# Kernel tuning notes

Measured on AMD Instinct MI355X. Metric: run time of the kernel, lower is better.

The kernel has to match this reference:

```python
import jax, jax.numpy as jnp
import numpy as np
from jax import lax

NUM_C = 100
EMB = 256
B = 64
L = 500
NSTU = 4096
N = NUM_C + 1  # skill_embedding rows / GCN node count


def gcn_conv(x, src, dst, W, b):
    # PyG GCNConv: add self-loops, symmetric deg^-1/2 norm, scatter-add at target.
    # x: [N, Fin]; src, dst: [E] (duplicates kept, as in PyG); W: [Fout, Fin]
    n = x.shape[0]
    loop = jnp.arange(n)
    s = jnp.concatenate([src, loop])
    d = jnp.concatenate([dst, loop])
    deg = jnp.zeros((n,), x.dtype).at[d].add(1.0)
    dinv = jnp.where(deg > 0, lax.rsqrt(deg), 0.0)
    norm = dinv[s] * dinv[d]  # [E+N]
    h = x @ W.T
    out = jnp.zeros((n, h.shape[1]), x.dtype).at[d].add(norm[:, None] * h[s])
    return out + b


def rnn(x, Wih, Whh, bih, bhh):
    # torch.nn.RNN (tanh, batch_first): h_t = tanh(x_t Wih^T + bih + h_{t-1} Whh^T + bhh)
    h0 = jnp.zeros((x.shape[0], Whh.shape[0]), x.dtype)
    def step(h, xt):
        h = jnp.tanh(xt @ Wih.T + bih + h @ Whh.T + bhh)
        return h, h
    _, hs = lax.scan(step, h0, jnp.swapaxes(x, 0, 1))
    return jnp.swapaxes(hs, 0, 1)


def next_pred(res, skill):
    # (res * one_hot(next_skill)).sum(-1); row NUM_C of the one-hot table is all-zero padding
    ns = skill[:, 1:]
    p = jnp.take_along_axis(res, jnp.minimum(ns, NUM_C - 1)[..., None], axis=-1)[..., 0]
    return jnp.where(ns == NUM_C, 0.0, p)


def _forward(student, skill, answer, G, skill_emb, answer_emb, stu,
             hg_w1, hg_b1, hg_w2, hg_b2, gcn_w1, gcn_b1, gcn_w2, gcn_b2,
             w1_w, w1_b, w2_w, w2_b, fc_d_w, fc_d_b, fc_h_w, fc_h_b,
             fc_e_w, fc_e_b, pos, dg_wih, dg_whh, dg_bih, dg_bhh,
             hgr_wih, hgr_whh, hgr_bih, hgr_bhh):
    mask = (answer != 2)[..., None].astype(jnp.float32)  # [B,L,1]
    src, dst = skill[:, :-1], skill[:, 1:]               # per-sample edge lists [B,L-1]

    # HGNN over student hypergraph (eval mode: dropout = identity): x' = G (x W + b)
    h = jax.nn.relu(G @ (stu @ hg_w1.T + hg_b1))
    stu_embedding = G @ (h @ hg_w2.T + hg_b2)            # [NSTU, EMB]

    se = skill_emb[skill]                                # [B,L,EMB]
    ae = answer_emb[answer]
    skill_answer = jnp.concatenate([se, ae], -1)
    answer_skill = jnp.concatenate([ae, se], -1)
    stu_h = stu_embedding[student - 1]                   # one_hot @ table == gather, [B,L,EMB]

    # per-sample 2-layer GCN over the shared skill embedding table, vmapped over batch
    gcn2 = jax.vmap(lambda s, d: gcn_conv(
        jax.nn.relu(gcn_conv(skill_emb, s, d, gcn_w1, gcn_b1)), s, d, gcn_w2, gcn_b2))
    all_h = gcn2(src, dst)                               # [B,N,EMB]

    g = jnp.take_along_axis(all_h, skill[..., None], axis=1) * mask  # [B,L,EMB]
    lengths = mask.sum(axis=1)[:, 0].astype(jnp.int32)   # effective lengths [B]
    expand_pos = pos[lengths - 1]                        # [B,L,1] (L==500)
    expand_pos = jax.nn.softmax(expand_pos * mask, axis=1)
    pooled = (g * expand_pos).sum(axis=1)                # [B,EMB]
    pooled = jnp.broadcast_to(pooled[:, None, :], (B, L, EMB))

    x = jnp.where((answer == 1)[..., None], skill_answer, answer_skill)  # [B,L,2E]
    h_dg = rnn(jnp.concatenate([pooled, x], -1), dg_wih, dg_whh, dg_bih, dg_bhh)
    h_hg = rnn(jnp.concatenate([stu_h, x], -1), hgr_wih, hgr_whh, hgr_bih, hgr_bhh)

    logit_h = h_hg @ fc_h_w.T + fc_h_b
    logit_d = h_dg @ fc_d_w.T + fc_d_b
    theta = jax.nn.sigmoid(h_hg @ w1_w.T + w1_b + h_dg @ w2_w.T + w2_b)
    ens = jnp.concatenate([theta * h_hg, (1.0 - theta) * h_dg], -1) @ fc_e_w.T + fc_e_b
    return (next_pred(logit_h[:, :-1], skill),
            next_pred(logit_d[:, :-1], skill),
            next_pred(ens[:, :-1], skill))


def setup_inputs() -> dict:
    key = jax.random.key(0)
    ks = jax.random.split(key, 24)
    f = lambda i, shape, s=0.05: jax.random.normal(ks[i], shape, jnp.float32) * s
    return {
        "student": jax.random.randint(ks[0], (B, L), 1, NSTU + 1),
        "skill": jax.random.randint(ks[1], (B, L), 0, N),
        "answer": jax.random.randint(ks[2], (B, L), 0, 3),
        "G": f(3, (NSTU, NSTU), 0.01),
        "skill_emb": f(4, (N, EMB), 1.0),
        "answer_emb": f(5, (3, EMB), 1.0),
        "stu": f(6, (NSTU, EMB), 1.0),
        "hg_w1": f(7, (EMB, EMB)), "hg_b1": jnp.zeros((EMB,), jnp.float32),
        "hg_w2": f(8, (EMB, EMB)), "hg_b2": jnp.zeros((EMB,), jnp.float32),
        "gcn_w1": f(9, (8, EMB)), "gcn_b1": jnp.zeros((8,), jnp.float32),
        "gcn_w2": f(10, (EMB, 8)), "gcn_b2": jnp.zeros((EMB,), jnp.float32),
        "w1_w": f(11, (EMB, EMB)), "w1_b": jnp.zeros((EMB,), jnp.float32),
        "w2_w": f(12, (EMB, EMB)), "w2_b": jnp.zeros((EMB,), jnp.float32),
        "fc_d_w": f(13, (NUM_C, EMB)), "fc_d_b": jnp.zeros((NUM_C,), jnp.float32),
        "fc_h_w": f(14, (NUM_C, EMB)), "fc_h_b": jnp.zeros((NUM_C,), jnp.float32),
        "fc_e_w": f(15, (NUM_C, 2 * EMB)), "fc_e_b": jnp.zeros((NUM_C,), jnp.float32),
        "pos": jax.random.uniform(ks[16], (500, 500, 1), jnp.float32),
        "dg_wih": f(17, (EMB, 3 * EMB)), "dg_whh": f(18, (EMB, EMB)),
        "dg_bih": jnp.zeros((EMB,), jnp.float32), "dg_bhh": jnp.zeros((EMB,), jnp.float32),
        "hgr_wih": f(19, (EMB, 3 * EMB)), "hgr_whh": f(20, (EMB, EMB)),
        "hgr_bih": jnp.zeros((EMB,), jnp.float32), "hgr_bhh": jnp.zeros((EMB,), jnp.float32),
    }


def reference(student, skill, answer, G, skill_emb, answer_emb, stu,
              hg_w1, hg_b1, hg_w2, hg_b2, gcn_w1, gcn_b1, gcn_w2, gcn_b2,
              w1_w, w1_b, w2_w, w2_b, fc_d_w, fc_d_b, fc_h_w, fc_h_b,
              fc_e_w, fc_e_b, pos, dg_wih, dg_whh, dg_bih, dg_bhh,
              hgr_wih, hgr_whh, hgr_bih, hgr_bhh):
    return _forward(student, skill, answer, G, skill_emb, answer_emb, stu,
                    hg_w1, hg_b1, hg_w2, hg_b2, gcn_w1, gcn_b1, gcn_w2, gcn_b2,
                    w1_w, w1_b, w2_w, w2_b, fc_d_w, fc_d_b, fc_h_w, fc_h_b,
                    fc_e_w, fc_e_b, pos, dg_wih, dg_whh, dg_bih, dg_bhh,
                    hgr_wih, hgr_whh, hgr_bih, hgr_bhh)
```

## Files before the change

kernel.cpp:

```cpp
#include <hip/hip_runtime.h>
#include <cstdint>
#include <cstddef>

typedef unsigned short u16;
typedef __attribute__((ext_vector_type(8))) short short8;
typedef __attribute__((ext_vector_type(4))) short short4v;
typedef __attribute__((ext_vector_type(4))) float f32x4;

__device__ __forceinline__ float b2f(u16 u){ return __uint_as_float(((unsigned)u)<<16); }
__device__ __forceinline__ u16 f2b(float f){
    unsigned u = __float_as_uint(f);
    return (u16)((u + 0x7fffu + ((u>>16)&1u)) >> 16);
}
__device__ __forceinline__ int iclamp(int v, int lo, int hi){ return v<lo?lo:(v>hi?hi:v); }

__device__ __forceinline__ void barrier_lds(){
    asm volatile("s_waitcnt lgkmcnt(0)\n\ts_barrier" ::: "memory");
}

__device__ __forceinline__ float fast_exp2(float x){
#if __has_builtin(__builtin_amdgcn_exp2f)
    return __builtin_amdgcn_exp2f(x);
#else
    return __expf(x * 0.6931471805599453f);
#endif
}

__device__ __forceinline__ short8 ld8f(const float* p){
    f32x4 a = *(const f32x4*)p;
    f32x4 b = *(const f32x4*)(p+4);
    short8 r;
    #pragma unroll
    for(int j=0;j<4;j++){ r[j]=(short)f2b(a[j]); r[4+j]=(short)f2b(b[j]); }
    return r;
}
__device__ __forceinline__ short8 ld8f_s(const float* p, float s){
    f32x4 a = *(const f32x4*)p;
    f32x4 b = *(const f32x4*)(p+4);
    short8 r;
    #pragma unroll
    for(int j=0;j<4;j++){ r[j]=(short)f2b(a[j]*s); r[4+j]=(short)f2b(b[j]*s); }
    return r;
}
__device__ __forceinline__ short8 ld8b(const u16* p){ return *(const short8*)p; }

#define C_TANH 2.8853900817779268f

template<bool TRANSOUT, bool RELU, bool AF32, bool BF32>
__global__ __launch_bounds__(256) void gemm64(
    const void* __restrict__ A, const void* __restrict__ B,
    const float* __restrict__ bias, u16* __restrict__ C,
    int M, int N, int K, int ldb, int ldc)
{
    constexpr int BK=32;
    __shared__ u16 As[2][64][BK+8];
    __shared__ u16 Bs[2][64][BK+8];
    const int tid = threadIdx.x;
    const int bm = blockIdx.x*64, bn = blockIdx.y*64;
    const int wave = tid>>6, lane = tid&63, lm = lane&15, lg = lane>>4;
    const int wm = (wave>>1)*32, wn = (wave&1)*32;
    f32x4 acc[2][2];
    #pragma unroll
    for(int i=0;i<2;i++){ acc[i][0]=(f32x4){0.f,0.f,0.f,0.f}; acc[i][1]=(f32x4){0.f,0.f,0.f,0.f}; }

    const int arow = tid>>2, akc = (tid&3)*8;
    auto lda8 = [&](int k)->short8{
        return AF32 ? ld8f((const float*)A + (size_t)(bm+arow)*K + k+akc)
                    : ld8b((const u16*)A + (size_t)(bm+arow)*K + k+akc);
    };
    auto ldb8v = [&](int k)->short8{
        return BF32 ? ld8f((const float*)B + (size_t)(bn+arow)*ldb + k+akc)
                    : ld8b((const u16*)B + (size_t)(bn+arow)*ldb + k+akc);
    };
    *(short8*)&As[0][arow][akc] = lda8(0);
    *(short8*)&Bs[0][arow][akc] = ldb8v(0);
    short8 a_hold, b_hold;
    if(BK < K){ a_hold = lda8(BK); b_hold = ldb8v(BK); }
    barrier_lds();
    int p = 0;
    for(int k0=0;k0<K;k0+=BK){
        short8 a_next, b_next;
        const bool have2 = (k0+2*BK < K);
        if(have2){ a_next = lda8(k0+2*BK); b_next = ldb8v(k0+2*BK); }
        short8 af[2], bfg[2];
        #pragma unroll
        for(int mt=0;mt<2;mt++) af[mt]  = *(const short8*)&As[p][wm+mt*16+lm][lg*8];
        #pragma unroll
        for(int nt=0;nt<2;nt++) bfg[nt] = *(const short8*)&Bs[p][wn+nt*16+lm][lg*8];
        if(k0+BK < K){
            *(short8*)&As[p^1][arow][akc] = a_hold;
            *(short8*)&Bs[p^1][arow][akc] = b_hold;
        }
        #pragma unroll
        for(int nt=0;nt<2;nt++)
            #pragma unroll
            for(int mt=0;mt<2;mt++)
                acc[mt][nt] = __builtin_amdgcn_mfma_f32_16x16x32_bf16(af[mt], bfg[nt], acc[mt][nt], 0,0,0);
        barrier_lds();
        a_hold = a_next; b_hold = b_next;
        p ^= 1;
    }
    #pragma unroll
    for(int nt=0;nt<2;nt++){
        const int col = bn+wn+nt*16+lm;
        const float bv = bias ? bias[col] : 0.f;
        #pragma unroll
        for(int mt=0;mt<2;mt++){
            const int row0 = bm+wm+mt*16+lg*4;
            #pragma unroll
            for(int r=0;r<4;r++){
                const int row = row0+r;
                float v = acc[mt][nt][r] + bv;
                if(RELU) v = fmaxf(v, 0.f);
                const size_t idx = TRANSOUT ? ((size_t)col*ldc + row) : ((size_t)row*ldc + col);
                C[idx] = f2b(v);
            }
        }
    }
}

__global__ __launch_bounds__(256) void k_prep(
    const float* __restrict__ skill_emb, const float* __restrict__ answer_emb,
    const float* __restrict__ wih_dg, const float* __restrict__ bih_dg, const float* __restrict__ bhh_dg,
    const float* __restrict__ wih_hg, const float* __restrict__ bih_hg, const float* __restrict__ bhh_hg,
    const float* __restrict__ gcn_w1,
    const int* __restrict__ skill, const int* __restrict__ answer, const int* __restrict__ student,
    const float* __restrict__ G, u16* __restrict__ Gb,
    float* __restrict__ table_dg, float* __restrict__ table_hg,
    float* __restrict__ h1pre, int* __restrict__ combo_t, int* __restrict__ sid_t)
{
    const int bid = blockIdx.x, tid = threadIdx.x;
    if(bid < 606){
        const int which = (bid >= 303) ? 1 : 0;
        const int combo = bid - which*303;
        const float* wih = which ? wih_hg : wih_dg;
        const float* bih = which ? bih_hg : bih_dg;
        const float* bhh = which ? bhh_hg : bhh_dg;
        float* table     = which ? table_hg : table_dg;
        const int sid = combo/3, ans = combo - sid*3;
        __shared__ float sf[256], sg[256];
        sf[tid] = (ans==1) ? skill_emb[(size_t)sid*256+tid] : answer_emb[(size_t)ans*256+tid];
        sg[tid] = (ans==1) ? answer_emb[(size_t)ans*256+tid] : skill_emb[(size_t)sid*256+tid];
        __syncthreads();
        const int o = tid;
        float acc = bih[o] + bhh[o];
        const float* w = wih + (size_t)o*768;
        for(int k=0;k<256;k+=4){
            f32x4 w1v = *(const f32x4*)&w[256+k];
            f32x4 w2v = *(const f32x4*)&w[512+k];
            acc += sf[k]*w1v.x + sf[k+1]*w1v.y + sf[k+2]*w1v.z + sf[k+3]*w1v.w;
            acc += sg[k]*w2v.x + sg[k+1]*w2v.y + sg[k+2]*w2v.z + sg[k+3]*w2v.w;
        }
        table[(size_t)combo*256 + o] = acc;
    } else if(bid < 731){
        const int i = (bid-606)*256 + tid;
        if(i>=32000) return;
        const int t = i>>6, b = i&63;
        const int sk = iclamp(skill[b*500+t], 0, 100);
        const int an = iclamp(answer[b*500+t], 0, 2);
        const int sd = iclamp(student[b*500+t]-1, 0, 4095);
        combo_t[i] = sk*3+an;
        sid_t[i]   = sd;
    } else if(bid < 739){
        if(tid >= 101) return;
        const int idx = (bid-731)*101 + tid;
        if(idx>=808) return;
        const int n=idx>>3, j=idx&7;
        const float* x = skill_emb + n*256;
        const float* w = gcn_w1 + j*256;
        float acc=0.f;
        for(int k=0;k<256;k+=4){
            f32x4 a = *(const f32x4*)&x[k];
            f32x4 b = *(const f32x4*)&w[k];
            acc += a.x*b.x + a.y*b.y + a.z*b.z + a.w*b.w;
        }
        h1pre[idx]=acc;
    } else {
        const size_t i = ((size_t)(bid-739)*256 + tid)*8;
        *(short8*)&Gb[i] = ld8f(G + i);
    }
}

__global__ __launch_bounds__(256) void k_gcn(
    const int* __restrict__ skill, const int* __restrict__ answer,
    const float* __restrict__ pos, const float* __restrict__ h1pre,
    const float* __restrict__ gcn_b1, const float* __restrict__ gcn_w2, const float* __restrict__ gcn_b2,
    const float* __restrict__ wih_dg,
    u16* __restrict__ pooled_proj)
{
    const int b = blockIdx.x, tid = threadIdx.x;
    __shared__ int   sk[500];
    __shared__ float msk[500];
    __shared__ float coef[500];
    __shared__ float deg[101];
    __shared__ float agg1[101*8];
    __shared__ float agg2[101*8];
    __shared__ float red[256];
    __shared__ float vec8[8];
    __shared__ float sS[1];

    for(int i=tid;i<500;i+=256){
        sk[i]=iclamp(skill[b*500+i],0,100);
        msk[i] = (answer[b*500+i]!=2)?1.f:0.f;
    }
    for(int i=tid;i<101;i+=256) deg[i]=1.f;
    if(tid<8)  vec8[tid]=0.f;
    if(tid==8) sS[0]=0.f;
    __syncthreads();
    for(int e=tid;e<499;e+=256) atomicAdd(&deg[sk[e+1]], 1.f);
    __syncthreads();
    for(int i=tid;i<101;i+=256) deg[i] = rsqrtf(deg[i]);
    float cnt=0.f; for(int i=tid;i<500;i+=256) cnt += msk[i];
    __syncthreads();
    red[tid]=cnt; __syncthreads();
    for(int s=128;s>0;s>>=1){ if(tid<s) red[tid]+=red[tid+s]; __syncthreads(); }
    const int len = iclamp((int)(red[0]+0.5f), 1, 500);
    __syncthreads();
    for(int i=tid;i<808;i+=256){ const int n=i>>3; agg1[i] = deg[n]*deg[n]*h1pre[i]; }
    __syncthreads();
    for(int i=tid;i<499*8;i+=256){
        const int e=i>>3, j=i&7, s=sk[e], d=sk[e+1];
        atomicAdd(&agg1[d*8+j], deg[s]*deg[d]*h1pre[s*8+j]);
    }
    __syncthreads();
    for(int i=tid;i<808;i+=256){ const int j=i&7; agg1[i] = fmaxf(agg1[i]+gcn_b1[j], 0.f); }
    __syncthreads();
    for(int i=tid;i<808;i+=256){ const int n=i>>3; agg2[i] = deg[n]*deg[n]*agg1[i]; }
    __syncthreads();
    for(int i=tid;i<499*8;i+=256){
        const int e=i>>3, j=i&7, s=sk[e], d=sk[e+1];
        atomicAdd(&agg2[d*8+j], deg[s]*deg[d]*agg1[s*8+j]);
    }
    const size_t prow = (size_t)(len-1)*500;
    float vmax = -1e30f;
    for(int i=tid;i<500;i+=256){ const float v = pos[prow+i]*msk[i]; coef[i]=v; vmax=fmaxf(vmax,v); }
    red[tid]=vmax; __syncthreads();
    for(int s=128;s>0;s>>=1){ if(tid<s) red[tid]=fmaxf(red[tid],red[tid+s]); __syncthreads(); }
    const float m = red[0]; __syncthreads();
    float lsum=0.f;
    for(int i=tid;i<500;i+=256){ const float e=__expf(coef[i]-m); coef[i]=e; lsum+=e; }
    red[tid]=lsum; __syncthreads();
    for(int s=128;s>0;s>>=1){ if(tid<s) red[tid]+=red[tid+s]; __syncthreads(); }
    const float inv = 1.f/red[0];
    __syncthreads();
    float v8[8]={0,0,0,0,0,0,0,0}; float ls=0.f;
    for(int i=tid;i<500;i+=256){
        const float ci = coef[i]*inv*msk[i];
        if(ci!=0.f){
            const int n=sk[i]; ls+=ci;
            #pragma unroll
            for(int j=0;j<8;j++) v8[j] += ci*agg2[n*8+j];
        }
    }
    #pragma unroll
    for(int j=0;j<8;j++) atomicAdd(&vec8[j], v8[j]);
    atomicAdd(&sS[0], ls);
    __syncthreads();
    {
        const int o = tid;
        float acc = gcn_b2[o]*sS[0];
        #pragma unroll
        for(int j=0;j<8;j++) acc += vec8[j]*gcn_w2[o*8+j];
        red[o] = acc;
    }
    __syncthreads();
    {
        const int o = tid;
        const float* w = wih_dg + (size_t)o*768;
        float acc=0.f;
        for(int k=0;k<256;k+=4){
            f32x4 wv = *(const f32x4*)&w[k];
            acc += red[k]*wv.x + red[k+1]*wv.y + red[k+2]*wv.z + red[k+3]*wv.w;
        }
        pooled_proj[b*256+o]=f2b(acc);
    }
}

__global__ __launch_bounds__(256) void k_pre(
    const int* __restrict__ combo_t, const int* __restrict__ sid_t,
    const float* __restrict__ table_dg, const float* __restrict__ table_hg,
    const u16* __restrict__ pooled_proj, const u16* __restrict__ stu_proj,
    u16* __restrict__ pre_dg, u16* __restrict__ pre_hg)
{
    const int t = blockIdx.x, rnn = blockIdx.y, c = threadIdx.x;
    const int b0 = blockIdx.z*16;
    const float* tab = rnn ? table_hg : table_dg;
    u16* outp = rnn ? pre_hg : pre_dg;
    for(int b=b0;b<b0+16;b++){
        const int cmb = combo_t[t*64+b];
        const u16* prow = rnn ? (stu_proj + (size_t)sid_t[t*64+b]*256)
                              : (pooled_proj + (size_t)b*256);
        const float v = (tab[(size_t)cmb*256 + c] + b2f(prow[c])) * C_TANH;
        outp[((size_t)t*64+b)*256 + c] = f2b(v);
    }
}

__global__ __launch_bounds__(1024) void k_rnn(
    const u16* __restrict__ pre_dg, const u16* __restrict__ pre_hg,
    const float* __restrict__ whh_dg, const float* __restrict__ whh_hg,
    u16* __restrict__ hall_dg, u16* __restrict__ hall_hg)
{
    __shared__ u16 hc[2][8][4][16][8];
    const int bid = blockIdx.x;
    const int rnn = bid>>2, grp = bid&3, rb = grp*16;
    const float* W   = rnn ? whh_hg : whh_dg;
    const u16*  pre  = rnn ? pre_hg : pre_dg;
    u16*        out  = rnn ? hall_hg : hall_dg;
    const int tid = threadIdx.x, wave = tid>>6, lane = tid&63;
    const int lm = lane&15, lg = lane>>4;
    const int cb = wave*16;

    short8 wf[8];
    #pragma unroll
    for(int kk=0;kk<8;kk++)
        wf[kk] = ld8f_s(W + (size_t)(cb+lm)*256 + kk*32 + lg*8, C_TANH);

    for(int i=tid;i<2*8*4*16*8/2;i+=1024) ((unsigned*)hc)[i]=0;

    const size_t base = (size_t)(rb+lm)*256 + cb + lg*4;
    const int wchunk = wave>>1, wsub = (wave&1)*2 + (lg>>1), wslot = (lg&1)*4;

    const u16* pp = pre + base;
    u16*       op = out + base;
    uint2 pv = *(const uint2*)pp;
    pp += 16384;
    __syncthreads();

    auto stepf = [&](const u16 (&S)[8][4][16][8], u16 (&D)[8][4][16][8],
                     uint2 pvi, const u16* ppi, u16* opi)->uint2 {
        f32x4 a0, c0 = (f32x4){0.f,0.f,0.f,0.f};
        a0[0] = __uint_as_float(pvi.x << 16);
        a0[1] = __uint_as_float(pvi.x & 0xffff0000u);
        a0[2] = __uint_as_float(pvi.y << 16);
        a0[3] = __uint_as_float(pvi.y & 0xffff0000u);
        #pragma unroll
        for(int kk=0;kk<4;kk++){
            short8 hb = *(const short8*)&S[kk][lg][lm][0];
            a0 = __builtin_amdgcn_mfma_f32_16x16x32_bf16(wf[kk], hb, a0, 0,0,0);
        }
        #pragma unroll
        for(int kk=4;kk<8;kk++){
            short8 hb = *(const short8*)&S[kk][lg][lm][0];
            c0 = __builtin_amdgcn_mfma_f32_16x16x32_bf16(wf[kk], hb, c0, 0,0,0);
        }
        const uint2 pvn = *(const uint2*)ppi;
        float th[4];
        #pragma unroll
        for(int r=0;r<4;r++){
            const float x = a0[r] + c0[r];
            const float e = fast_exp2(x);
            th[r] = fmaf(-2.f, __builtin_amdgcn_rcpf(e + 1.f), 1.f);
        }
        uint2 pk;
        asm("v_cvt_pk_bf16_f32 %0, %1, %2" : "=v"(pk.x) : "v"(th[0]), "v"(th[1]));
        asm("v_cvt_pk_bf16_f32 %0, %1, %2" : "=v"(pk.y) : "v"(th[2]), "v"(th[3]));
        *(uint2*)&D[wchunk][wsub][lm][wslot] = pk;
        *(uint2*)opi = pk;
        barrier_lds();
        return pvn;
    };

    for(int t=0;t<500;t+=2){
        pv = stepf(hc[0], hc[1], pv, pp, op);  pp += 16384; op += 16384;
        pv = stepf(hc[1], hc[0], pv, pp, op);  pp += 16384; op += 16384;
    }
}

__global__ __launch_bounds__(256) void k_theta(
    const u16* __restrict__ Ah, const u16* __restrict__ Ad,
    const float* __restrict__ w1, const float* __restrict__ w2,
    const float* __restrict__ b1, const float* __restrict__ b2,
    u16* __restrict__ theta)
{
    constexpr int BK=32;
    __shared__ u16 AsH[128][BK+8];
    __shared__ u16 AsD[128][BK+8];
    __shared__ u16 BsH[64][BK+8];
    __shared__ u16 BsD[64][BK+8];
    const int tid = threadIdx.x;
    const int bm = blockIdx.x*128, bn = blockIdx.y*64;
    const int wave = tid>>6, lane = tid&63, lm = lane&15, lg = lane>>4;
    const int wm = (wave>>1)*64, wn = (wave&1)*32;
    f32x4 acc[4][2];
    #pragma unroll
    for(int i=0;i<4;i++){ acc[i][0]=(f32x4){0.f,0.f,0.f,0.f}; acc[i][1]=(f32x4){0.f,0.f,0.f,0.f}; }

    const int arow0 = tid>>2, akc0 = (tid&3)*8;
    const int arow1 = arow0 + 64;
    for(int k0=0;k0<256;k0+=BK){
        *(short8*)&AsH[arow0][akc0] = ld8b(Ah + (size_t)(bm+arow0)*256 + k0+akc0);
        *(short8*)&AsH[arow1][akc0] = ld8b(Ah + (size_t)(bm+arow1)*256 + k0+akc0);
        *(short8*)&AsD[arow0][akc0] = ld8b(Ad + (size_t)(bm+arow0)*256 + k0+akc0);
        *(short8*)&AsD[arow1][akc0] = ld8b(Ad + (size_t)(bm+arow1)*256 + k0+akc0);
        *(short8*)&BsH[arow0][akc0] = ld8f(w1 + (size_t)(bn+arow0)*256 + k0+akc0);
        *(short8*)&BsD[arow0][akc0] = ld8f(w2 + (size_t)(bn+arow0)*256 + k0+akc0);
        __syncthreads();
        short8 afH[4], afD[4], bf1[2], bf2[2];
        #pragma unroll
        for(int mt=0;mt<4;mt++){
            afH[mt] = *(const short8*)&AsH[wm+mt*16+lm][lg*8];
            afD[mt] = *(const short8*)&AsD[wm+mt*16+lm][lg*8];
        }
        #pragma unroll
        for(int nt=0;nt<2;nt++){
            bf1[nt] = *(const short8*)&BsH[wn+nt*16+lm][lg*8];
            bf2[nt] = *(const short8*)&BsD[wn+nt*16+lm][lg*8];
        }
        #pragma unroll
        for(int nt=0;nt<2;nt++)
            #pragma unroll
            for(int mt=0;mt<4;mt++){
                acc[mt][nt] = __builtin_amdgcn_mfma_f32_16x16x32_bf16(afH[mt], bf1[nt], acc[mt][nt], 0,0,0);
                acc[mt][nt] = __builtin_amdgcn_mfma_f32_16x16x32_bf16(afD[mt], bf2[nt], acc[mt][nt], 0,0,0);
            }
        __syncthreads();
    }
    #pragma unroll
    for(int nt=0;nt<2;nt++){
        const int col = bn+wn+nt*16+lm;
        const float bb = b1[col]+b2[col];
        #pragma unroll
        for(int mt=0;mt<4;mt++){
            const int row0 = bm+wm+mt*16+lg*4;
            #pragma unroll
            for(int r=0;r<4;r++){
                const float x = acc[mt][nt][r] + bb;
                theta[(size_t)(row0+r)*256 + col] = f2b(1.f/(1.f+__expf(-x)));
            }
        }
    }
}

__global__ __launch_bounds__(256) void k_out(
    const int* __restrict__ skill,
    const u16* __restrict__ hall_hg, const u16* __restrict__ hall_dg,
    const u16* __restrict__ theta,
    const float* __restrict__ fc_h_w, const float* __restrict__ fc_h_b,
    const float* __restrict__ fc_d_w, const float* __restrict__ fc_d_b,
    const float* __restrict__ fc_e_w, const float* __restrict__ fc_e_b,
    float* __restrict__ outp)
{
    const int tid=threadIdx.x, lane=tid&63;
    const int wid = blockIdx.x*4 + (tid>>6);
    const int b = wid/499, t = wid - b*499;
    const int ns = skill[b*500 + t + 1];
    float o0=0.f,o1=0.f,o2=0.f,bh=0.f,bd=0.f,be=0.f;
    if(ns != 100){
        const int c = iclamp(ns, 0, 99);
        const size_t r = (size_t)t*64 + b;
        const int k = lane*4;
        short4v hh  = *(const short4v*)&hall_hg[r*256+k];
        short4v hd  = *(const short4v*)&hall_dg[r*256+k];
        short4v th  = *(const short4v*)&theta[r*256+k];
        f32x4 fh  = *(const f32x4*)&fc_h_w[(size_t)c*256+k];
        f32x4 fd  = *(const f32x4*)&fc_d_w[(size_t)c*256+k];
        f32x4 fe1 = *(const f32x4*)&fc_e_w[(size_t)c*512+k];
        f32x4 fe2 = *(const f32x4*)&fc_e_w[(size_t)c*512+256+k];
        #pragma unroll
        for(int j=0;j<4;j++){
            const float hhj=b2f((u16)hh[j]), hdj=b2f((u16)hd[j]), tj=b2f((u16)th[j]);
            o0 += hhj*fh[j];
            o1 += hdj*fd[j];
            o2 += tj*hhj*fe1[j] + (1.f-tj)*hdj*fe2[j];
        }
        #pragma unroll
        for(int off=32;off>0;off>>=1){
            o0 += __shfl_down(o0,off);
            o1 += __shfl_down(o1,off);
            o2 += __shfl_down(o2,off);
        }
        bh=fc_h_b[c]; bd=fc_d_b[c]; be=fc_e_b[c];
    }
    if(lane==0){
        outp[            b*499+t] = (ns==100)?0.f:(o0+bh);
        outp[31936     + b*499+t] = (ns==100)?0.f:(o1+bd);
        outp[2*31936   + b*499+t] = (ns==100)?0.f:(o2+be);
    }
}

extern "C" void kernel_launch(void* const* d_in, const int* in_sizes, int n_in,
                              void* d_out, int out_size, void* d_ws, size_t ws_size,
                              hipStream_t stream)
{
    const int* student = (const int*)d_in[0];
    const int* skill   = (const int*)d_in[1];
    const int* answer  = (const int*)d_in[2];
    const float* G        = (const float*)d_in[3];
    const float* skill_emb= (const float*)d_in[4];
    const float* answer_emb=(const float*)d_in[5];
    const float* stu      = (const float*)d_in[6];
    const float* hg_w1    = (const float*)d_in[7];
    const float* hg_b1    = (const float*)d_in[8];
    const float* hg_w2    = (const float*)d_in[9];
    const float* hg_b2    = (const float*)d_in[10];
    const float* gcn_w1   = (const float*)d_in[11];
    const float* gcn_b1   = (const float*)d_in[12];
    const float* gcn_w2   = (const float*)d_in[13];
    const float* gcn_b2   = (const float*)d_in[14];
    const float* w1_w     = (const float*)d_in[15];
    const float* w1_b     = (const float*)d_in[16];
    const float* w2_w     = (const float*)d_in[17];
    const float* w2_b     = (const float*)d_in[18];
    const float* fc_d_w   = (const float*)d_in[19];
    const float* fc_d_b   = (const float*)d_in[20];
    const float* fc_h_w   = (const float*)d_in[21];
    const float* fc_h_b   = (const float*)d_in[22];
    const float* fc_e_w   = (const float*)d_in[23];
    const float* fc_e_b   = (const float*)d_in[24];
    const float* pos      = (const float*)d_in[25];
    const float* dg_wih   = (const float*)d_in[26];
    const float* dg_whh   = (const float*)d_in[27];
    const float* dg_bih   = (const float*)d_in[28];
    const float* dg_bhh   = (const float*)d_in[29];
    const float* hgr_wih  = (const float*)d_in[30];
    const float* hgr_whh  = (const float*)d_in[31];
    const float* hgr_bih  = (const float*)d_in[32];
    const float* hgr_bhh  = (const float*)d_in[33];

    char* ws = (char*)d_ws;
    size_t off = 0;
    auto nxt = [&](size_t bytes)->char*{
        char* r = ws + off;
        off += (bytes + 255) & ~(size_t)255;
        return r;
    };
    float* h1pre      = (float*)nxt(808*4);
    float* table_dg   = (float*)nxt(303*256*4);
    float* table_hg   = (float*)nxt(303*256*4);
    u16*   tmpT       = (u16*)  nxt((size_t)256*4096*2);
    u16*   hbuf       = (u16*)  nxt((size_t)4096*256*2);
    u16*   stu_proj   = (u16*)  nxt((size_t)4096*256*2);
    u16*   pooled_proj= (u16*)  nxt(64*256*2);
    int*   combo_t    = (int*)  nxt(32000*4);
    int*   sid_t      = (int*)  nxt(32000*4);
    u16*   Gb         = (u16*)  nxt((size_t)4096*4096*2);
    u16*   hall_dg    = (u16*)  nxt((size_t)32000*256*2);
    u16*   hall_hg    = (u16*)  nxt((size_t)32000*256*2);
    u16*   pre_dg     = Gb;
    u16*   pre_hg     = Gb + (size_t)32000*256;
    u16*   theta      = pre_dg;

    k_prep<<<8931,256,0,stream>>>(skill_emb, answer_emb,
                                  dg_wih, dg_bih, dg_bhh,
                                  hgr_wih, hgr_bih, hgr_bhh,
                                  gcn_w1, skill, answer, student,
                                  G, Gb,
                                  table_dg, table_hg, h1pre, combo_t, sid_t);
    k_gcn<<<64,256,0,stream>>>(skill, answer, pos, h1pre, gcn_b1, gcn_w2, gcn_b2,
                               dg_wih, pooled_proj);

    gemm64<true ,false,true ,true ><<<dim3(64,4),256,0,stream>>>(stu,  hg_w1, hg_b1, tmpT, 4096,256,256,  256, 4096);
    gemm64<false,true ,false,false><<<dim3(64,4),256,0,stream>>>(Gb,   tmpT,  nullptr, hbuf, 4096,256,4096, 4096, 256);
    gemm64<true ,false,false,true ><<<dim3(64,4),256,0,stream>>>(hbuf, hg_w2, hg_b2, tmpT, 4096,256,256,  256, 4096);
    gemm64<false,false,false,false><<<dim3(64,4),256,0,stream>>>(Gb,   tmpT,  nullptr, hbuf, 4096,256,4096, 4096, 256);
    gemm64<false,false,false,true ><<<dim3(64,4),256,0,stream>>>(hbuf, hgr_wih, nullptr, stu_proj, 4096,256,256, 768, 256);

    k_pre<<<dim3(500,2,4),256,0,stream>>>(combo_t, sid_t, table_dg, table_hg,
                                          pooled_proj, stu_proj, pre_dg, pre_hg);

    k_rnn<<<8,1024,0,stream>>>(pre_dg, pre_hg, dg_whh, hgr_whh, hall_dg, hall_hg);

    k_theta<<<dim3(250,4),256,0,stream>>>(hall_hg, hall_dg, w1_w, w2_w, w1_b, w2_b, theta);
    k_out<<<7984,256,0,stream>>>(skill, hall_hg, hall_dg, theta,
                                 fc_h_w, fc_h_b, fc_d_w, fc_d_b, fc_e_w, fc_e_b,
                                 (float*)d_out);
}
```

Baseline: 789.6 us.

## Fuse HGNN GEMM chain and pre-activation gather into one persistent kernel

Replaces the five separate GEMM launches and the k_pre launch with a single 256-block persistent kernel. Stages are separated by a global atomic-counter barrier, and the counter is reset inside k_prep. The intent is to remove kernel launch gaps and tail effects between the dependent stages. In exchange, the pre-activation gather now runs as a 250-iteration serial loop per block instead of thousands of blocks, which cuts latency hiding. The global barrier also relies on all 256 blocks being co-resident on the device.

```diff
diff --git a/kernel.cpp b/kernel.cpp
--- a/kernel.cpp
+++ b/kernel.cpp
@@ -46,17 +46,29 @@
 
 #define C_TANH 2.8853900817779268f
 
+__device__ __forceinline__ void gsync(unsigned* cnt, unsigned target){
+    __syncthreads();
+    __threadfence();
+    if(threadIdx.x==0){
+        atomicAdd(cnt, 1u);
+        while(__hip_atomic_load(cnt, __ATOMIC_RELAXED, __HIP_MEMORY_SCOPE_AGENT) < target){
+            __builtin_amdgcn_s_sleep(2);
+        }
+    }
+    __syncthreads();
+    __threadfence();
+}
+
 template<bool TRANSOUT, bool RELU, bool AF32, bool BF32>
-__global__ __launch_bounds__(256) void gemm64(
+__device__ __forceinline__ void gemm_dev(
     const void* __restrict__ A, const void* __restrict__ B,
     const float* __restrict__ bias, u16* __restrict__ C,
-    int M, int N, int K, int ldb, int ldc)
+    int M, int N, int K, int ldb, int ldc, int bx, int by,
+    u16 (&As)[2][64][40], u16 (&Bs)[2][64][40])
 {
     constexpr int BK=32;
-    __shared__ u16 As[2][64][BK+8];
-    __shared__ u16 Bs[2][64][BK+8];
     const int tid = threadIdx.x;
-    const int bm = blockIdx.x*64, bn = blockIdx.y*64;
+    const int bm = bx*64, bn = by*64;
     const int wave = tid>>6, lane = tid&63, lm = lane&15, lg = lane>>4;
     const int wm = (wave>>1)*32, wn = (wave&1)*32;
     f32x4 acc[2][2];
@@ -119,6 +131,49 @@
     }
 }
 
+__global__ __launch_bounds__(256) void k_mega(
+    const float* __restrict__ stu, const float* __restrict__ hg_w1, const float* __restrict__ hg_b1,
+    const u16* __restrict__ Gb, const float* __restrict__ hg_w2, const float* __restrict__ hg_b2,
+    const float* __restrict__ hgr_wih,
+    u16* __restrict__ tmpT, u16* __restrict__ hbuf, u16* __restrict__ stu_proj,
+    const int* __restrict__ combo_t, const int* __restrict__ sid_t,
+    const float* __restrict__ table_dg, const float* __restrict__ table_hg,
+    const u16* __restrict__ pooled_proj,
+    u16* __restrict__ pre_dg, u16* __restrict__ pre_hg,
+    unsigned* __restrict__ cnt)
+{
+    __shared__ u16 As[2][64][40];
+    __shared__ u16 Bs[2][64][40];
+    const int bid = blockIdx.x;
+    const int bx = bid & 63, by = bid >> 6;
+
+    gemm_dev<true ,false,true ,true >(stu,  hg_w1, hg_b1, tmpT, 4096,256,256,  256, 4096, bx,by, As,Bs);
+    gsync(cnt, 256);
+    gemm_dev<false,true ,false,false>(Gb,   tmpT,  nullptr, hbuf, 4096,256,4096, 4096, 256, bx,by, As,Bs);
+    gsync(cnt, 512);
+    gemm_dev<true ,false,false,true >(hbuf, hg_w2, hg_b2, tmpT, 4096,256,256,  256, 4096, bx,by, As,Bs);
+    gsync(cnt, 768);
+    gemm_dev<false,false,false,false>(Gb,   tmpT,  nullptr, hbuf, 4096,256,4096, 4096, 256, bx,by, As,Bs);
+    gsync(cnt, 1024);
+    gemm_dev<false,false,false,true >(hbuf, hgr_wih, nullptr, stu_proj, 4096,256,256, 768, 256, bx,by, As,Bs);
+    gsync(cnt, 1280);
+
+    const int c = threadIdx.x;
+    int tt = bid*250;
+    int rnn = tt/32000, r = tt - rnn*32000;
+    for(int i=0;i<250;i++){
+        const int t = r>>6, b = r&63;
+        const int cmb = combo_t[t*64+b];
+        const float* tab = rnn ? table_hg : table_dg;
+        const u16* prow = rnn ? (stu_proj + (size_t)sid_t[t*64+b]*256)
+                              : (pooled_proj + (size_t)b*256);
+        u16* outp = rnn ? pre_hg : pre_dg;
+        const float v = (tab[(size_t)cmb*256 + c] + b2f(prow[c])) * C_TANH;
+        outp[((size_t)t*64+b)*256 + c] = f2b(v);
+        if(++r == 32000){ r = 0; rnn = 1; }
+    }
+}
+
 __global__ __launch_bounds__(256) void k_prep(
     const float* __restrict__ skill_emb, const float* __restrict__ answer_emb,
     const float* __restrict__ wih_dg, const float* __restrict__ bih_dg, const float* __restrict__ bhh_dg,
@@ -127,9 +182,11 @@
     const int* __restrict__ skill, const int* __restrict__ answer, const int* __restrict__ student,
     const float* __restrict__ G, u16* __restrict__ Gb,
     float* __restrict__ table_dg, float* __restrict__ table_hg,
-    float* __restrict__ h1pre, int* __restrict__ combo_t, int* __restrict__ sid_t)
+    float* __restrict__ h1pre, int* __restrict__ combo_t, int* __restrict__ sid_t,
+    unsigned* __restrict__ cnt)
 {
     const int bid = blockIdx.x, tid = threadIdx.x;
+    if(bid==0 && tid==0) *cnt = 0u;
     if(bid < 606){
         const int which = (bid >= 303) ? 1 : 0;
         const int combo = bid - which*303;
@@ -273,25 +330,6 @@
             acc += red[k]*wv.x + red[k+1]*wv.y + red[k+2]*wv.z + red[k+3]*wv.w;
         }
         pooled_proj[b*256+o]=f2b(acc);
-    }
-}
-
-__global__ __launch_bounds__(256) void k_pre(
-    const int* __restrict__ combo_t, const int* __restrict__ sid_t,
-    const float* __restrict__ table_dg, const float* __restrict__ table_hg,
-    const u16* __restrict__ pooled_proj, const u16* __restrict__ stu_proj,
-    u16* __restrict__ pre_dg, u16* __restrict__ pre_hg)
-{
-    const int t = blockIdx.x, rnn = blockIdx.y, c = threadIdx.x;
-    const int b0 = blockIdx.z*16;
-    const float* tab = rnn ? table_hg : table_dg;
-    u16* outp = rnn ? pre_hg : pre_dg;
-    for(int b=b0;b<b0+16;b++){
-        const int cmb = combo_t[t*64+b];
-        const u16* prow = rnn ? (stu_proj + (size_t)sid_t[t*64+b]*256)
-                              : (pooled_proj + (size_t)b*256);
-        const float v = (tab[(size_t)cmb*256 + c] + b2f(prow[c])) * C_TANH;
-        outp[((size_t)t*64+b)*256 + c] = f2b(v);
     }
 }
 
@@ -533,6 +571,7 @@
     u16*   pooled_proj= (u16*)  nxt(64*256*2);
     int*   combo_t    = (int*)  nxt(32000*4);
     int*   sid_t      = (int*)  nxt(32000*4);
+    unsigned* cnt     = (unsigned*)nxt(256);
     u16*   Gb         = (u16*)  nxt((size_t)4096*4096*2);
     u16*   hall_dg    = (u16*)  nxt((size_t)32000*256*2);
     u16*   hall_hg    = (u16*)  nxt((size_t)32000*256*2);
@@ -545,18 +584,14 @@
                                   hgr_wih, hgr_bih, hgr_bhh,
                                   gcn_w1, skill, answer, student,
                                   G, Gb,
-                                  table_dg, table_hg, h1pre, combo_t, sid_t);
+                                  table_dg, table_hg, h1pre, combo_t, sid_t, cnt);
     k_gcn<<<64,256,0,stream>>>(skill, answer, pos, h1pre, gcn_b1, gcn_w2, gcn_b2,
                                dg_wih, pooled_proj);
 
-    gemm64<true ,false,true ,true ><<<dim3(64,4),256,0,stream>>>(stu,  hg_w1, hg_b1, tmpT, 4096,256,256,  256, 4096);
-    gemm64<false,true ,false,false><<<dim3(64,4),256,0,stream>>>(Gb,   tmpT,  nullptr, hbuf, 4096,256,4096, 4096, 256);
-    gemm64<true ,false,false,true ><<<dim3(64,4),256,0,stream>>>(hbuf, hg_w2, hg_b2, tmpT, 4096,256,256,  256, 4096);
-    gemm64<false,false,false,false><<<dim3(64,4),256,0,stream>>>(Gb,   tmpT,  nullptr, hbuf, 4096,256,4096, 4096, 256);
-    gemm64<false,false,false,true ><<<dim3(64,4),256,0,stream>>>(hbuf, hgr_wih, nullptr, stu_proj, 4096,256,256, 768, 256);
-
-    k_pre<<<dim3(500,2,4),256,0,stream>>>(combo_t, sid_t, table_dg, table_hg,
-                                          pooled_proj, stu_proj, pre_dg, pre_hg);
+    k_mega<<<256,256,0,stream>>>(stu, hg_w1, hg_b1, Gb, hg_w2, hg_b2, hgr_wih,
+                                 tmpT, hbuf, stu_proj,
+                                 combo_t, sid_t, table_dg, table_hg, pooled_proj,
+                                 pre_dg, pre_hg, cnt);
 
     k_rnn<<<8,1024,0,stream>>>(pre_dg, pre_hg, dg_whh, hgr_whh, hall_dg, hall_hg);
 
```

Measured after the change: 1.069 ms. +35.4%, slower.
